# Kernel tuning notes

Measured on AMD Instinct MI355X. Metric: run time of the kernel, lower is better.

The kernel has to match this reference:

```python
import jax, jax.numpy as jnp
import numpy as np

HOP = 240  # subsample stride from torch.arange(239, T, 240)

def _causal_conv(x, w, b):
    # x: [B, Cin, T], w: [Cout, Cin, K], b: [Cout]
    pad = w.shape[-1] - 1
    xp = jnp.pad(x, ((0, 0), (0, 0), (pad, 0)))
    y = jax.lax.conv_general_dilated(xp, w, window_strides=(1,), padding='VALID',
                                     dimension_numbers=('NCW', 'OIW', 'NCW'))
    return y + b[None, :, None], xp[:, :, -pad:]

def _rvq(z, codebooks):
    # z: [B, T, D]; codebooks: [n, codebook_size, cd] with D = n*cd
    B, T, D = z.shape
    n, cs, cd = codebooks.shape
    zc = z.reshape(B, T, n, cd)
    r = zc[:, :, 0, :]
    qs, idxs = [], []
    for i in range(n):  # fixed small loop over 8 codebooks (sequential residual chain)
        cb = codebooks[i]  # [cs, cd]
        dist = (r ** 2).sum(-1, keepdims=True) + (cb ** 2).sum(-1) \
               - 2.0 * jnp.einsum('btd,cd->btc', r, cb)
        idx = jnp.argmin(dist, axis=-1)  # [B, T]
        q = cb[idx]                      # [B, T, cd]
        idxs.append(idx)
        qs.append(q)
        if i < n - 1:
            r = zc[:, :, i + 1, :] + (r - q)
    z_q = jnp.stack(qs, axis=2).reshape(B, T, D)
    return z_q, jnp.stack(idxs, axis=1)  # indices: [B, n, T]

def setup_inputs() -> dict:
    key = jax.random.key(0)
    ks = jax.random.split(key, 12)
    B, T = 4, 72000
    d_model = 512
    n_cb, cb_size, cb_dim = 8, 1024, d_model // 8
    s = 0.05
    return {
        'audio':   jax.random.normal(ks[0], (B, 1, T), dtype=jnp.float32),
        'conv1_w': jax.random.normal(ks[1], (64, 1, 7), dtype=jnp.float32) * s,
        'conv1_b': jnp.zeros((64,), dtype=jnp.float32),
        'conv2_w': jax.random.normal(ks[2], (128, 64, 5), dtype=jnp.float32) * s,
        'conv2_b': jnp.zeros((128,), dtype=jnp.float32),
        'conv3_w': jax.random.normal(ks[3], (256, 128, 5), dtype=jnp.float32) * s,
        'conv3_b': jnp.zeros((256,), dtype=jnp.float32),
        'conv4_w': jax.random.normal(ks[4], (d_model, 256, 3), dtype=jnp.float32) * s,
        'conv4_b': jnp.zeros((d_model,), dtype=jnp.float32),
        'codebooks': jax.random.normal(ks[5], (n_cb, cb_size, cb_dim), dtype=jnp.float32),
        'head_w': jax.random.normal(ks[6], (4, 64, d_model), dtype=jnp.float32) * s,
        'head_b': jnp.zeros((4, 64), dtype=jnp.float32),
    }

def reference(audio, conv1_w, conv1_b, conv2_w, conv2_b, conv3_w, conv3_b,
              conv4_w, conv4_b, codebooks, head_w, head_b):
    x, s1 = _causal_conv(audio, conv1_w, conv1_b); x = jax.nn.elu(x)
    x, s2 = _causal_conv(x, conv2_w, conv2_b);     x = jax.nn.elu(x)
    x, s3 = _causal_conv(x, conv3_w, conv3_b);     x = jax.nn.elu(x)
    x, s4 = _causal_conv(x, conv4_w, conv4_b);     x = jax.nn.elu(x)
    idx = jnp.arange(HOP - 1, x.shape[-1], HOP)
    x_sub = jnp.take(x, idx, axis=-1)              # [B, D, T_sub]
    z_q, a_tokens = _rvq(jnp.transpose(x_sub, (0, 2, 1)), codebooks)
    # b_logits: [B, 4, T_sub, 64]
    b_logits = jnp.einsum('btd,hod->bhto', z_q, head_w) + head_b[None, :, None, :]
    return a_tokens, b_logits, s1, s2, s3, s4
```

## Files before the change

kernel.cpp:

```cpp
#include <hip/hip_runtime.h>
#include <math.h>

#define HOP   240
#define T_IN  72000
#define NB    4
#define NF    300
#define NCB   8
#define CBS   1024
#define CBD   64

#define OFF_LOG 9600
#define OFF_S1  316800
#define OFF_S2  316824
#define OFF_S3  317848
#define OFF_S4  319896

#define WS_NRM   0
#define WS_W2P4  8192
#define WS_W3P4  49152
#define WS_W4P4  212992
#define WS_HW4   606208
#define WS_CBP4  737280
#define WS_TOTAL 1261568ull

__device__ __forceinline__ float elu1(float x) { return x > 0.f ? x : expm1f(x); }
__device__ __forceinline__ float dot4(float4 a, float4 b) {
    return a.x * b.x + a.y * b.y + a.z * b.z + a.w * b.w;
}
__device__ __forceinline__ float red16(float v) {
    v += __shfl_xor(v, 1); v += __shfl_xor(v, 2);
    v += __shfl_xor(v, 4); v += __shfl_xor(v, 8);
    return v;
}
__device__ __forceinline__ unsigned int fkey(float f) {
    unsigned int u = __float_as_uint(f);
    return (u & 0x80000000u) ? ~u : (u | 0x80000000u);
}

__global__ __launch_bounds__(256)
void prep_kernel(const float* __restrict__ w2, const float* __restrict__ w3,
                 const float* __restrict__ w4, const float* __restrict__ hw,
                 const float* __restrict__ cbs, float* __restrict__ wsf)
{
    const int bid = blockIdx.x;
    const float* src; float* dst;
    int R, L, I, K, tix, cx;
    bool do_norm = false;
    float* nrmp = nullptr;
    if (bid < 10)       { src = w2; dst = wsf + WS_W2P4; R = 128; L = 320; I = 64;  K = 5; tix = bid;       cx = 5;  }
    else if (bid < 50)  { src = w3; dst = wsf + WS_W3P4; R = 256; L = 640; I = 128; K = 5; tix = bid - 10;  cx = 10; }
    else if (bid < 146) { src = w4; dst = wsf + WS_W4P4; R = 512; L = 768; I = 256; K = 3; tix = bid - 50;  cx = 12; }
    else if (bid < 178) { src = hw; dst = wsf + WS_HW4;  R = 256; L = 512; I = 512; K = 1; tix = bid - 146; cx = 8;  }
    else {
        const int e = bid - 178, book = e >> 4;
        src = cbs + (size_t)book * 65536; dst = wsf + WS_CBP4 + (size_t)book * 65536;
        R = 1024; L = 64; I = 64; K = 1; tix = e & 15; cx = 1;
        do_norm = true; nrmp = wsf + WS_NRM + book * 1024;
    }
    const int c0 = (tix % cx) * 64, r0 = (tix / cx) * 64;
    const int lane = threadIdx.x & 63, q = threadIdx.x >> 6;

    __shared__ float tS[64][65];
    __shared__ float npart[4][64];

    #pragma unroll
    for (int i = 0; i < 16; ++i) {
        const int rr = q * 16 + i;
        tS[rr][lane] = src[(size_t)(r0 + rr) * L + c0 + lane];
    }
    __syncthreads();

    if (do_norm) {
        float s = 0.f;
        #pragma unroll
        for (int j = 0; j < 16; ++j) { const float v = tS[lane][q * 16 + j]; s += v * v; }
        npart[q][lane] = s;
        __syncthreads();
        if (threadIdx.x < 64)
            nrmp[r0 + threadIdx.x] = npart[0][threadIdx.x] + npart[1][threadIdx.x]
                                   + npart[2][threadIdx.x] + npart[3][threadIdx.x];
    }

    #pragma unroll
    for (int i = 0; i < 16; ++i) {
        const int col = c0 + q * 16 + i;
        const int dr = (K == 1) ? col : (col % K) * I + col / K;
        dst[((size_t)(dr >> 2) * R + (r0 + lane)) * 4 + (dr & 3)] = tS[lane][q * 16 + i];
    }
}

__global__ __launch_bounds__(512)
void mega_kernel(const float* __restrict__ audio,
                 const float* __restrict__ w1, const float* __restrict__ b1,
                 const float* __restrict__ b2, const float* __restrict__ b3,
                 const float* __restrict__ b4, const float* __restrict__ cbs,
                 const float* __restrict__ hb, const float* __restrict__ wsf,
                 float* __restrict__ out)
{
    const int blk = blockIdx.x;
    const int b   = blk / 60;
    const int f0  = (blk - b * 60) * 5;
    const int tid = threadIdx.x;
    const int lane = tid & 63, wid = tid >> 6;

    __shared__ float ashL[5][18];
    __shared__ __align__(16) float y1L[5 * 704];
    __shared__ __align__(16) float y2L[5 * 896];
    __shared__ __align__(16) float y3L[5 * 768];
    __shared__ __align__(16) float zsL[5 * 512];
    __shared__ __align__(16) float zqL[5 * 512];
    __shared__ __align__(16) float rs[320];
    __shared__ float redL[4480];
    __shared__ float rnS[5];
    __shared__ unsigned long long mk[2][5];

    if (tid < 85) {
        const int f = tid / 17, j = tid - (tid / 17) * 17;
        ashL[f][j] = audio[b * T_IN + (f0 + f) * HOP + 223 + j];
    }
    if (blk == 239 && tid < 6) out[OFF_S1 + 3 * 6 + tid] = audio[3 * T_IN + (T_IN - 6) + tid];
    __syncthreads();

    if (tid < 320) {
        const int f = tid >> 6, o = tid & 63;
        float wv[7];
        #pragma unroll
        for (int k = 0; k < 7; ++k) wv[k] = w1[o * 7 + k];
        const float bias = b1[o];
        float y1r[11];
        #pragma unroll
        for (int p = 0; p < 11; ++p) {
            float a = bias;
            #pragma unroll
            for (int k = 0; k < 7; ++k) a += wv[k] * ashL[f][p + k];
            y1r[p] = elu1(a);
            y1L[f * 704 + p * 64 + o] = y1r[p];
        }
        if (blk == 239 && f == 4) {
            #pragma unroll
            for (int j = 0; j < 4; ++j) out[OFF_S2 + 3 * 256 + o * 4 + j] = y1r[7 + j];
        }
    }
    __syncthreads();

    {
        const int c = tid & 127, h = (tid >> 7) & 1, g = tid >> 8;
        const int fb = g ? 3 : 0, nf = g ? 2 : 3;
        float acc[3][7];
        #pragma unroll
        for (int ff = 0; ff < 3; ++ff)
            #pragma unroll
            for (int p = 0; p < 7; ++p) acc[ff][p] = 0.f;

        const float4* wq = (const float4*)(wsf + WS_W2P4);
        for (int it = 0; it < 8; ++it) {
            const int itg = h * 8 + it;
            float4 wv[5];
            #pragma unroll
            for (int k = 0; k < 5; ++k) wv[k] = wq[(k * 16 + itg) * 128 + c];
            #pragma unroll
            for (int q = 0; q < 11; ++q) {
                float4 xv[3];
                #pragma unroll
                for (int ff = 0; ff < 3; ++ff)
                    if (ff < nf) xv[ff] = *(const float4*)&y1L[(fb + ff) * 704 + q * 64 + itg * 4];
                #pragma unroll
                for (int k = 0; k < 5; ++k) {
                    const int p = q - k;
                    if (p < 0 || p > 6) continue;
                    #pragma unroll
                    for (int ff = 0; ff < 3; ++ff)
                        if (ff < nf) acc[ff][p] += dot4(wv[k], xv[ff]);
                }
            }
        }
        if (h == 1) {
            #pragma unroll
            for (int ff = 0; ff < 3; ++ff)
                if (ff < nf)
                    #pragma unroll
                    for (int p = 0; p < 7; ++p)
                        redL[((fb + ff) * 7 + p) * 128 + c] = acc[ff][p];
        }
        __syncthreads();
        if (h == 0) {
            const float bias = b2[c];
            #pragma unroll
            for (int ff = 0; ff < 3; ++ff)
                if (ff < nf) {
                    const int f = fb + ff;
                    #pragma unroll
                    for (int p = 0; p < 7; ++p) {
                        const float v = elu1(acc[ff][p] + redL[(f * 7 + p) * 128 + c] + bias);
                        y2L[f * 896 + p * 128 + c] = v;
                        if (blk == 239 && f == 4 && p >= 3)
                            out[OFF_S3 + 3 * 512 + c * 4 + (p - 3)] = v;
                    }
                }
        }
        __syncthreads();
    }

    {
        const int c = tid & 255, h = tid >> 8;
        float acc[5][3];
        #pragma unroll
        for (int ff = 0; ff < 5; ++ff) { acc[ff][0] = acc[ff][1] = acc[ff][2] = 0.f; }

        const float4* wq = (const float4*)(wsf + WS_W3P4);
        for (int it = 0; it < 16; ++it) {
            const int itg = h * 16 + it;
            float4 wv[5];
            #pragma unroll
            for (int k = 0; k < 5; ++k) wv[k] = wq[(k * 32 + itg) * 256 + c];
            #pragma unroll
            for (int q = 0; q < 7; ++q) {
                float4 xv[5];
                #pragma unroll
                for (int ff = 0; ff < 5; ++ff)
                    xv[ff] = *(const float4*)&y2L[ff * 896 + q * 128 + itg * 4];
                #pragma unroll
                for (int k = 0; k < 5; ++k) {
                    const int p = q - k;
                    if (p < 0 || p > 2) continue;
                    #pragma unroll
                    for (int ff = 0; ff < 5; ++ff) acc[ff][p] += dot4(wv[k], xv[ff]);
                }
            }
        }
        if (h == 1) {
            #pragma unroll
            for (int ff = 0; ff < 5; ++ff)
                #pragma unroll
                for (int p = 0; p < 3; ++p) redL[(ff * 3 + p) * 256 + c] = acc[ff][p];
        }
        __syncthreads();
        if (h == 0) {
            const float bias = b3[c];
            #pragma unroll
            for (int ff = 0; ff < 5; ++ff)
                #pragma unroll
                for (int p = 0; p < 3; ++p) {
                    const float v = elu1(acc[ff][p] + redL[(ff * 3 + p) * 256 + c] + bias);
                    y3L[ff * 768 + p * 256 + c] = v;
                    if (blk == 239 && ff == 4 && p >= 1)
                        out[OFF_S4 + 3 * 512 + c * 2 + (p - 1)] = v;
                }
        }
        __syncthreads();
    }

    if (tid < 256) {
        const int c0 = tid, c1 = tid + 256;
        float a0[5], a1[5];
        #pragma unroll
        for (int ff = 0; ff < 5; ++ff) { a0[ff] = 0.f; a1[ff] = 0.f; }
        const float4* wq = (const float4*)(wsf + WS_W4P4);
        for (int rc = 0; rc < 192; ++rc) {
            const float4 w0 = wq[rc * 512 + c0];
            const float4 w1v = wq[rc * 512 + c1];
            #pragma unroll
            for (int ff = 0; ff < 5; ++ff) {
                const float4 xv = *(const float4*)&y3L[ff * 768 + rc * 4];
                a0[ff] += dot4(w0, xv);
                a1[ff] += dot4(w1v, xv);
            }
        }
        const float bi0 = b4[c0], bi1 = b4[c1];
        #pragma unroll
        for (int ff = 0; ff < 5; ++ff) {
            zsL[ff * 512 + c0] = elu1(a0[ff] + bi0);
            zsL[ff * 512 + c1] = elu1(a1[ff] + bi1);
        }
    }
    if (tid < 10) mk[tid / 5][tid % 5] = ~0ull;
    __syncthreads();

    if (tid < 320) {
        const float v = zsL[wid * 512 + lane];
        rs[tid] = v;
        float ss = v * v;
        #pragma unroll
        for (int m = 1; m < 64; m <<= 1) ss += __shfl_xor(ss, m);
        if (lane == 0) rnS[wid] = ss;
    }
    __syncthreads();

    const int c0 = tid << 1;
    for (int s = 0; s < NCB; ++s) {
        const float4* cbq = (const float4*)(wsf + WS_CBP4) + (size_t)s * 16384;
        float dA[5], dB[5];
        #pragma unroll
        for (int ff = 0; ff < 5; ++ff) { dA[ff] = 0.f; dB[ff] = 0.f; }

        for (int dc = 0; dc < 16; ++dc) {
            const float4 la = cbq[dc * 1024 + c0];
            const float4 lb = cbq[dc * 1024 + c0 + 1];
            #pragma unroll
            for (int ff = 0; ff < 5; ++ff) {
                const float4 rv = *(const float4*)&rs[ff * 64 + dc * 4];
                dA[ff] += dot4(la, rv);
                dB[ff] += dot4(lb, rv);
            }
        }
        const float2 nn = *(const float2*)(wsf + WS_NRM + s * CBS + c0);
        unsigned long long key[5];
        #pragma unroll
        for (int ff = 0; ff < 5; ++ff) {
            const float rn = rnS[ff];
            const float da = (rn + nn.x) - 2.f * dA[ff];
            const float db = (rn + nn.y) - 2.f * dB[ff];
            const unsigned long long ka = ((unsigned long long)fkey(da) << 32) | (unsigned)c0;
            const unsigned long long kb = ((unsigned long long)fkey(db) << 32) | (unsigned)(c0 + 1);
            key[ff] = ka < kb ? ka : kb;
        }
        #pragma unroll
        for (int m = 1; m < 64; m <<= 1) {
            #pragma unroll
            for (int ff = 0; ff < 5; ++ff) {
                const unsigned long long o = __shfl_xor(key[ff], m);
                if (o < key[ff]) key[ff] = o;
            }
        }
        if (lane == 0) {
            #pragma unroll
            for (int ff = 0; ff < 5; ++ff) atomicMin(&mk[s & 1][ff], key[ff]);
        }
        __syncthreads();

        if (tid < 5)
            out[b * (NCB * NF) + s * NF + (f0 + tid)]
                = (float)(unsigned)(mk[s & 1][tid] & 0xFFFFFFFFull);
        if (tid < 320) {
            const int idx = (int)(unsigned)(mk[s & 1][wid] & 0xFFFFFFFFull);
            const float qv = cbs[(size_t)(s * CBS + idx) * CBD + lane];
            zqL[wid * 512 + s * 64 + lane] = qv;
            if (s < NCB - 1) {
                const float nr = zsL[wid * 512 + (s + 1) * 64 + lane] + (rs[tid] - qv);
                rs[tid] = nr;
                float ss = nr * nr;
                #pragma unroll
                for (int m = 1; m < 64; m <<= 1) ss += __shfl_xor(ss, m);
                if (lane == 0) rnS[wid] = ss;
            }
        }
        if (tid >= 320 && tid < 325) mk[(s + 1) & 1][tid - 320] = ~0ull;
        __syncthreads();
    }

    {
        const int oc = tid & 255, h = tid >> 8;
        const float4* hq = (const float4*)(wsf + WS_HW4);
        float acc[5];
        #pragma unroll
        for (int ff = 0; ff < 5; ++ff) acc[ff] = 0.f;
        for (int rc = 0; rc < 64; ++rc) {
            const float4 wv = hq[(h * 64 + rc) * 256 + oc];
            #pragma unroll
            for (int ff = 0; ff < 5; ++ff) {
                const float4 xv = *(const float4*)&zqL[ff * 512 + h * 256 + rc * 4];
                acc[ff] += dot4(wv, xv);
            }
        }
        if (h == 1) {
            #pragma unroll
            for (int ff = 0; ff < 5; ++ff) redL[oc * 5 + ff] = acc[ff];
        }
        __syncthreads();
        if (h == 0) {
            const float bias = hb[oc];
            const int hh = oc >> 6, o = oc & 63;
            #pragma unroll
            for (int ff = 0; ff < 5; ++ff)
                out[OFF_LOG + ((size_t)(b * 4 + hh) * NF + (f0 + ff)) * 64 + o]
                    = acc[ff] + redL[oc * 5 + ff] + bias;
        }
    }
}

__global__ __launch_bounds__(256)
void enc_fused_kernel(const float* __restrict__ audio,
                      const float* __restrict__ w1, const float* __restrict__ b1,
                      const float* __restrict__ w2, const float* __restrict__ b2,
                      const float* __restrict__ w3, const float* __restrict__ b3,
                      const float* __restrict__ w4, const float* __restrict__ b4,
                      const float* __restrict__ cbs,
                      const float* __restrict__ hw, const float* __restrict__ hb,
                      float* __restrict__ out)
{
    const int tid = threadIdx.x;
    const int g = tid >> 4, sub = tid & 15, j0 = sub << 2;
    const int bf = blockIdx.x, b = bf / NF, f = bf - b * NF;
    const int t = f * HOP + (HOP - 1);

    __shared__ __align__(16) float ash[17];
    __shared__ __align__(16) float y1s[11 * 64];
    __shared__ __align__(16) float y2s[7 * 128];
    __shared__ __align__(16) float y3s[3 * 256];
    __shared__ __align__(16) float in_l[2240];
    __shared__ __align__(16) float zs[512];
    __shared__ __align__(16) float zqs[512];
    __shared__ __align__(16) float rsl[64];
    __shared__ float rdd[16]; __shared__ int rdi[16]; __shared__ int bidx_s;

    if (tid < 17) ash[tid] = audio[b * T_IN + (t - 16) + tid];
    __syncthreads();
    for (int j = tid; j < 11 * 64; j += 256) {
        const int p = j >> 6, o = j & 63;
        float acc = b1[o];
        for (int k = 0; k < 7; ++k) acc += w1[o * 7 + k] * ash[p + k];
        y1s[p * 64 + o] = elu1(acc);
    }
    __syncthreads();
    for (int j = tid; j < 7 * 320; j += 256) {
        const int p = j / 320, r = j - p * 320, i = r / 5, k = r - i * 5;
        in_l[j] = y1s[(p + k) * 64 + i];
    }
    __syncthreads();
    {
        float a[7];
        for (int ch = 0; ch < 8; ++ch) {
            const int c = g + (ch << 4);
            const float* wr = w2 + c * 320;
            for (int p = 0; p < 7; ++p) a[p] = 0.f;
            for (int st = 0; st < 5; ++st) {
                const float4 wv = *(const float4*)(wr + st * 64 + j0);
                for (int p = 0; p < 7; ++p)
                    a[p] += dot4(wv, *(const float4*)&in_l[p * 320 + st * 64 + j0]);
            }
            for (int p = 0; p < 7; ++p) a[p] = red16(a[p]);
            if (sub == 0) for (int p = 0; p < 7; ++p) y2s[p * 128 + c] = elu1(a[p] + b2[c]);
        }
    }
    __syncthreads();
    for (int j = tid; j < 3 * 640; j += 256) {
        const int p = j / 640, r = j - p * 640, i = r / 5, k = r - i * 5;
        in_l[j] = y2s[(p + k) * 128 + i];
    }
    __syncthreads();
    {
        float a[3];
        for (int ch = 0; ch < 16; ++ch) {
            const int c = g + (ch << 4);
            const float* wr = w3 + c * 640;
            a[0] = a[1] = a[2] = 0.f;
            for (int st = 0; st < 10; ++st) {
                const float4 wv = *(const float4*)(wr + st * 64 + j0);
                for (int p = 0; p < 3; ++p)
                    a[p] += dot4(wv, *(const float4*)&in_l[p * 640 + st * 64 + j0]);
            }
            for (int p = 0; p < 3; ++p) a[p] = red16(a[p]);
            if (sub == 0) for (int p = 0; p < 3; ++p) y3s[p * 256 + c] = elu1(a[p] + b3[c]);
        }
    }
    __syncthreads();
    for (int j = tid; j < 768; j += 256) { const int i = j / 3, k = j - i * 3; in_l[j] = y3s[k * 256 + i]; }
    __syncthreads();
    for (int ch = 0; ch < 32; ++ch) {
        const int c = g + (ch << 4);
        const float* wr = w4 + c * 768;
        float a = 0.f;
        for (int st = 0; st < 12; ++st)
            a += dot4(*(const float4*)(wr + st * 64 + j0), *(const float4*)&in_l[st * 64 + j0]);
        a = red16(a);
        if (sub == 0) zs[c] = elu1(a + b4[c]);
    }
    __syncthreads();
    if (tid < 64) rsl[tid] = zs[tid];
    __syncthreads();
    for (int s = 0; s < NCB; ++s) {
        const float* cb = cbs + s * (CBS * CBD);
        const float4 rv = *(const float4*)(rsl + j0);
        const float rn = red16(dot4(rv, rv));
        float bestd = 3.402823466e38f; int besti = 0;
        const int cc0 = g * 64;
        for (int cc = 0; cc < 64; ++cc) {
            const int c = cc0 + cc;
            const float4 cv = *(const float4*)(cb + c * CBD + j0);
            const float dt = red16(dot4(cv, rv));
            const float nnv = red16(dot4(cv, cv));
            const float d = rn + nnv - 2.f * dt;
            if (d < bestd) { bestd = d; besti = c; }
        }
        if (sub == 0) { rdd[g] = bestd; rdi[g] = besti; }
        __syncthreads();
        if (tid == 0) {
            float bd = rdd[0]; int bi = rdi[0];
            for (int q = 1; q < 16; ++q) if (rdd[q] < bd) { bd = rdd[q]; bi = rdi[q]; }
            bidx_s = bi;
            out[b * (NCB * NF) + s * NF + f] = (float)bi;
        }
        __syncthreads();
        const int idx = bidx_s;
        if (g == 0) {
            const float4 q4 = *(const float4*)(cb + idx * CBD + j0);
            *(float4*)&zqs[s * 64 + j0] = q4;
            if (s < NCB - 1) {
                const float4 zn = *(const float4*)&zs[(s + 1) * 64 + j0];
                float4 nr;
                nr.x = zn.x + (rv.x - q4.x); nr.y = zn.y + (rv.y - q4.y);
                nr.z = zn.z + (rv.z - q4.z); nr.w = zn.w + (rv.w - q4.w);
                *(float4*)&rsl[j0] = nr;
            }
        }
        __syncthreads();
    }
    for (int oo = 0; oo < 16; ++oo) {
        const int oc = g + (oo << 4);
        const float* wr = hw + oc * 512;
        float a = 0.f;
        for (int st = 0; st < 8; ++st)
            a += dot4(*(const float4*)(wr + st * 64 + j0), *(const float4*)&zqs[st * 64 + j0]);
        a = red16(a);
        if (sub == 0) {
            const int h = oc >> 6, o = oc & 63;
            out[OFF_LOG + ((b * 4 + h) * NF + f) * 64 + o] = a + hb[oc];
        }
    }
    if (f == NF - 1) {
        if (tid < 6) out[OFF_S1 + b * 6 + tid] = audio[b * T_IN + (T_IN - 6) + tid];
        out[OFF_S2 + b * 256 + tid] = y1s[(7 + (tid & 3)) * 64 + (tid >> 2)];
        for (int j = tid; j < 512; j += 256)
            out[OFF_S3 + b * 512 + j] = y2s[(3 + (j & 3)) * 128 + (j >> 2)];
        for (int j = tid; j < 512; j += 256)
            out[OFF_S4 + b * 512 + j] = y3s[(1 + (j & 1)) * 256 + (j >> 1)];
    }
}

extern "C" void kernel_launch(void* const* d_in, const int* in_sizes, int n_in,
                              void* d_out, int out_size, void* d_ws, size_t ws_size,
                              hipStream_t stream) {
    const float* audio = (const float*)d_in[0];
    const float* w1 = (const float*)d_in[1];
    const float* b1 = (const float*)d_in[2];
    const float* w2 = (const float*)d_in[3];
    const float* b2 = (const float*)d_in[4];
    const float* w3 = (const float*)d_in[5];
    const float* b3 = (const float*)d_in[6];
    const float* w4 = (const float*)d_in[7];
    const float* b4 = (const float*)d_in[8];
    const float* cbs = (const float*)d_in[9];
    const float* hw = (const float*)d_in[10];
    const float* hb = (const float*)d_in[11];
    float* out = (float*)d_out;
    float* wsf = (float*)d_ws;

    if (ws_size >= WS_TOTAL * sizeof(float)) {
        prep_kernel<<<dim3(306), 256, 0, stream>>>(w2, w3, w4, hw, cbs, wsf);
        mega_kernel<<<dim3(240), 512, 0, stream>>>(audio, w1, b1, b2, b3, b4,
                                                   cbs, hb, wsf, out);
    } else {
        enc_fused_kernel<<<dim3(NB * NF), 256, 0, stream>>>(
            audio, w1, b1, w2, b2, w3, b3, w4, b4, cbs, hw, hb, out);
    }
}
```

Before: 253.1 us.

## Shrink frames per block to three and rework prep weight repacking

```diff
diff --git a/kernel.cpp b/kernel.cpp
--- a/kernel.cpp
+++ b/kernel.cpp
@@ -44,52 +44,55 @@
 {
     const int bid = blockIdx.x;
     const float* src; float* dst;
-    int R, L, I, K, tix, cx;
-    bool do_norm = false;
-    float* nrmp = nullptr;
-    if (bid < 10)       { src = w2; dst = wsf + WS_W2P4; R = 128; L = 320; I = 64;  K = 5; tix = bid;       cx = 5;  }
-    else if (bid < 50)  { src = w3; dst = wsf + WS_W3P4; R = 256; L = 640; I = 128; K = 5; tix = bid - 10;  cx = 10; }
-    else if (bid < 146) { src = w4; dst = wsf + WS_W4P4; R = 512; L = 768; I = 256; K = 3; tix = bid - 50;  cx = 12; }
-    else if (bid < 178) { src = hw; dst = wsf + WS_HW4;  R = 256; L = 512; I = 512; K = 1; tix = bid - 146; cx = 8;  }
+    int C, I, K, c0, i0;
+    bool do_norm = false; float* nrmp = nullptr;
+    if (bid < 2)       { src = w2; dst = wsf + WS_W2P4; C = 128;  I = 64;  K = 5; c0 = bid * 64;        i0 = 0; }
+    else if (bid < 10) { const int e = bid - 2;  src = w3; dst = wsf + WS_W3P4; C = 256;  I = 128; K = 5; c0 = (e >> 1) * 64; i0 = (e & 1) * 64; }
+    else if (bid < 42) { const int e = bid - 10; src = w4; dst = wsf + WS_W4P4; C = 512;  I = 256; K = 3; c0 = (e >> 2) * 64; i0 = (e & 3) * 64; }
+    else if (bid < 74) { const int e = bid - 42; src = hw; dst = wsf + WS_HW4;  C = 256;  I = 512; K = 1; c0 = (e & 3) * 64;  i0 = (e >> 2) * 64; }
     else {
-        const int e = bid - 178, book = e >> 4;
+        const int e = bid - 74, book = e >> 4;
         src = cbs + (size_t)book * 65536; dst = wsf + WS_CBP4 + (size_t)book * 65536;
-        R = 1024; L = 64; I = 64; K = 1; tix = e & 15; cx = 1;
+        C = 1024; I = 64; K = 1; c0 = (e & 15) * 64; i0 = 0;
         do_norm = true; nrmp = wsf + WS_NRM + book * 1024;
     }
-    const int c0 = (tix % cx) * 64, r0 = (tix / cx) * 64;
+    const int L = I * K;
     const int lane = threadIdx.x & 63, q = threadIdx.x >> 6;
 
     __shared__ float tS[64][65];
     __shared__ float npart[4][64];
 
-    #pragma unroll
-    for (int i = 0; i < 16; ++i) {
-        const int rr = q * 16 + i;
-        tS[rr][lane] = src[(size_t)(r0 + rr) * L + c0 + lane];
-    }
-    __syncthreads();
-
-    if (do_norm) {
-        float s = 0.f;
-        #pragma unroll
-        for (int j = 0; j < 16; ++j) { const float v = tS[lane][q * 16 + j]; s += v * v; }
-        npart[q][lane] = s;
-        __syncthreads();
-        if (threadIdx.x < 64)
-            nrmp[r0 + threadIdx.x] = npart[0][threadIdx.x] + npart[1][threadIdx.x]
-                                   + npart[2][threadIdx.x] + npart[3][threadIdx.x];
-    }
-
-    #pragma unroll
-    for (int i = 0; i < 16; ++i) {
-        const int col = c0 + q * 16 + i;
-        const int dr = (K == 1) ? col : (col % K) * I + col / K;
-        dst[((size_t)(dr >> 2) * R + (r0 + lane)) * 4 + (dr & 3)] = tS[lane][q * 16 + i];
-    }
-}
-
-__global__ __launch_bounds__(512)
+    for (int k = 0; k < K; ++k) {
+        #pragma unroll
+        for (int r = 0; r < 16; ++r) {
+            const int cl = q * 16 + r;
+            tS[cl][lane] = src[(size_t)(c0 + cl) * L + (i0 + lane) * K + k];
+        }
+        __syncthreads();
+        if (do_norm && k == 0) {
+            float s = 0.f;
+            #pragma unroll
+            for (int j = 0; j < 16; ++j) { const float v = tS[lane][q * 16 + j]; s += v * v; }
+            npart[q][lane] = s;
+        }
+        #pragma unroll
+        for (int jj = 0; jj < 4; ++jj) {
+            const int j = q * 4 + jj;
+            float4 v;
+            v.x = tS[lane][4 * j + 0];
+            v.y = tS[lane][4 * j + 1];
+            v.z = tS[lane][4 * j + 2];
+            v.w = tS[lane][4 * j + 3];
+            ((float4*)dst)[(size_t)(k * (I >> 2) + (i0 >> 2) + j) * C + (c0 + lane)] = v;
+        }
+        __syncthreads();
+    }
+    if (do_norm && threadIdx.x < 64)
+        nrmp[c0 + threadIdx.x] = npart[0][threadIdx.x] + npart[1][threadIdx.x]
+                               + npart[2][threadIdx.x] + npart[3][threadIdx.x];
+}
+
+__global__ __launch_bounds__(512, 4)
 void mega_kernel(const float* __restrict__ audio,
                  const float* __restrict__ w1, const float* __restrict__ b1,
                  const float* __restrict__ b2, const float* __restrict__ b3,
@@ -98,30 +101,33 @@
                  float* __restrict__ out)
 {
     const int blk = blockIdx.x;
-    const int b   = blk / 60;
-    const int f0  = (blk - b * 60) * 5;
+    const int b   = blk / 100;
+    const int fi  = blk - b * 100;
+    const int f0  = fi * 3;
+    const bool tail = (fi == 99);
     const int tid = threadIdx.x;
     const int lane = tid & 63, wid = tid >> 6;
 
-    __shared__ float ashL[5][18];
-    __shared__ __align__(16) float y1L[5 * 704];
-    __shared__ __align__(16) float y2L[5 * 896];
-    __shared__ __align__(16) float y3L[5 * 768];
-    __shared__ __align__(16) float zsL[5 * 512];
-    __shared__ __align__(16) float zqL[5 * 512];
-    __shared__ __align__(16) float rs[320];
-    __shared__ float redL[4480];
-    __shared__ float rnS[5];
-    __shared__ unsigned long long mk[2][5];
-
-    if (tid < 85) {
-        const int f = tid / 17, j = tid - (tid / 17) * 17;
+    __shared__ float ashL[3][18];
+    __shared__ __align__(16) float y1L[3 * 704];
+    __shared__ __align__(16) float y2L[3 * 896];
+    __shared__ __align__(16) float y3L[3 * 768];
+    __shared__ __align__(16) float zsL[3 * 512];
+    __shared__ __align__(16) float zqL[3 * 512];
+    __shared__ __align__(16) float rs[192];
+    __shared__ float redL[2688];
+    __shared__ float rnS[3];
+    __shared__ unsigned long long mk[2][3];
+
+    if (tid < 51) {
+        const int f = tid / 17, j = tid - f * 17;
         ashL[f][j] = audio[b * T_IN + (f0 + f) * HOP + 223 + j];
     }
-    if (blk == 239 && tid < 6) out[OFF_S1 + 3 * 6 + tid] = audio[3 * T_IN + (T_IN - 6) + tid];
-    __syncthreads();
-
-    if (tid < 320) {
+    if (tail && tid < 6) out[OFF_S1 + b * 6 + tid] = audio[b * T_IN + (T_IN - 6) + tid];
+    if (tid < 6) mk[tid / 3][tid % 3] = ~0ull;
+    __syncthreads();
+
+    if (tid < 192) {
         const int f = tid >> 6, o = tid & 63;
         float wv[7];
         #pragma unroll
@@ -136,19 +142,19 @@
             y1r[p] = elu1(a);
             y1L[f * 704 + p * 64 + o] = y1r[p];
         }
-        if (blk == 239 && f == 4) {
-            #pragma unroll
-            for (int j = 0; j < 4; ++j) out[OFF_S2 + 3 * 256 + o * 4 + j] = y1r[7 + j];
+        if (tail && f == 2) {
+            #pragma unroll
+            for (int j = 0; j < 4; ++j) out[OFF_S2 + b * 256 + o * 4 + j] = y1r[7 + j];
         }
     }
     __syncthreads();
 
     {
         const int c = tid & 127, h = (tid >> 7) & 1, g = tid >> 8;
-        const int fb = g ? 3 : 0, nf = g ? 2 : 3;
-        float acc[3][7];
-        #pragma unroll
-        for (int ff = 0; ff < 3; ++ff)
+        const int fb = g * 2, nf = g ? 1 : 2;
+        float acc[2][7];
+        #pragma unroll
+        for (int ff = 0; ff < 2; ++ff)
             #pragma unroll
             for (int p = 0; p < 7; ++p) acc[ff][p] = 0.f;
 
@@ -160,23 +166,23 @@
             for (int k = 0; k < 5; ++k) wv[k] = wq[(k * 16 + itg) * 128 + c];
             #pragma unroll
             for (int q = 0; q < 11; ++q) {
-                float4 xv[3];
-                #pragma unroll
-                for (int ff = 0; ff < 3; ++ff)
+                float4 xv[2];
+                #pragma unroll
+                for (int ff = 0; ff < 2; ++ff)
                     if (ff < nf) xv[ff] = *(const float4*)&y1L[(fb + ff) * 704 + q * 64 + itg * 4];
                 #pragma unroll
                 for (int k = 0; k < 5; ++k) {
                     const int p = q - k;
                     if (p < 0 || p > 6) continue;
                     #pragma unroll
-                    for (int ff = 0; ff < 3; ++ff)
+                    for (int ff = 0; ff < 2; ++ff)
                         if (ff < nf) acc[ff][p] += dot4(wv[k], xv[ff]);
                 }
             }
         }
         if (h == 1) {
             #pragma unroll
-            for (int ff = 0; ff < 3; ++ff)
+            for (int ff = 0; ff < 2; ++ff)
                 if (ff < nf)
                     #pragma unroll
                     for (int p = 0; p < 7; ++p)
@@ -186,15 +192,15 @@
         if (h == 0) {
             const float bias = b2[c];
             #pragma unroll
-            for (int ff = 0; ff < 3; ++ff)
+            for (int ff = 0; ff < 2; ++ff)
                 if (ff < nf) {
                     const int f = fb + ff;
                     #pragma unroll
                     for (int p = 0; p < 7; ++p) {
                         const float v = elu1(acc[ff][p] + redL[(f * 7 + p) * 128 + c] + bias);
                         y2L[f * 896 + p * 128 + c] = v;
-                        if (blk == 239 && f == 4 && p >= 3)
-                            out[OFF_S3 + 3 * 512 + c * 4 + (p - 3)] = v;
+                        if (tail && f == 2 && p >= 3)
+                            out[OFF_S3 + b * 512 + c * 4 + (p - 3)] = v;
                     }
                 }
         }
@@ -203,9 +209,9 @@
 
     {
         const int c = tid & 255, h = tid >> 8;
-        float acc[5][3];
-        #pragma unroll
-        for (int ff = 0; ff < 5; ++ff) { acc[ff][0] = acc[ff][1] = acc[ff][2] = 0.f; }
+        float acc[3][3];
+        #pragma unroll
+        for (int ff = 0; ff < 3; ++ff) { acc[ff][0] = acc[ff][1] = acc[ff][2] = 0.f; }
 
         const float4* wq = (const float4*)(wsf + WS_W3P4);
         for (int it = 0; it < 16; ++it) {
@@ -215,22 +221,22 @@
             for (int k = 0; k < 5; ++k) wv[k] = wq[(k * 32 + itg) * 256 + c];
             #pragma unroll
             for (int q = 0; q < 7; ++q) {
-                float4 xv[5];
-                #pragma unroll
-                for (int ff = 0; ff < 5; ++ff)
+                float4 xv[3];
+                #pragma unroll
+                for (int ff = 0; ff < 3; ++ff)
                     xv[ff] = *(const float4*)&y2L[ff * 896 + q * 128 + itg * 4];
                 #pragma unroll
                 for (int k = 0; k < 5; ++k) {
                     const int p = q - k;
                     if (p < 0 || p > 2) continue;
                     #pragma unroll
-                    for (int ff = 0; ff < 5; ++ff) acc[ff][p] += dot4(wv[k], xv[ff]);
+                    for (int ff = 0; ff < 3; ++ff) acc[ff][p] += dot4(wv[k], xv[ff]);
                 }
             }
         }
         if (h == 1) {
             #pragma unroll
-            for (int ff = 0; ff < 5; ++ff)
+            for (int ff = 0; ff < 3; ++ff)
                 #pragma unroll
                 for (int p = 0; p < 3; ++p) redL[(ff * 3 + p) * 256 + c] = acc[ff][p];
         }
@@ -238,45 +244,38 @@
         if (h == 0) {
             const float bias = b3[c];
             #pragma unroll
-            for (int ff = 0; ff < 5; ++ff)
+            for (int ff = 0; ff < 3; ++ff)
                 #pragma unroll
                 for (int p = 0; p < 3; ++p) {
                     const float v = elu1(acc[ff][p] + redL[(ff * 3 + p) * 256 + c] + bias);
                     y3L[ff * 768 + p * 256 + c] = v;
-                    if (blk == 239 && ff == 4 && p >= 1)
-                        out[OFF_S4 + 3 * 512 + c * 2 + (p - 1)] = v;
+                    if (tail && ff == 2 && p >= 1)
+                        out[OFF_S4 + b * 512 + c * 2 + (p - 1)] = v;
                 }
         }
         __syncthreads();
     }
 
-    if (tid < 256) {
-        const int c0 = tid, c1 = tid + 256;
-        float a0[5], a1[5];
-        #pragma unroll
-        for (int ff = 0; ff < 5; ++ff) { a0[ff] = 0.f; a1[ff] = 0.f; }
+    {
+        const int c = tid;
+        float acc[3] = {0.f, 0.f, 0.f};
         const float4* wq = (const float4*)(wsf + WS_W4P4);
         for (int rc = 0; rc < 192; ++rc) {
-            const float4 w0 = wq[rc * 512 + c0];
-            const float4 w1v = wq[rc * 512 + c1];
-            #pragma unroll
-            for (int ff = 0; ff < 5; ++ff) {
+            const float4 w0 = wq[rc * 512 + c];
+            #pragma unroll
+            for (int ff = 0; ff < 3; ++ff) {
                 const float4 xv = *(const float4*)&y3L[ff * 768 + rc * 4];
-                a0[ff] += dot4(w0, xv);
-                a1[ff] += dot4(w1v, xv);
-            }
-        }
-        const float bi0 = b4[c0], bi1 = b4[c1];
-        #pragma unroll
-        for (int ff = 0; ff < 5; ++ff) {
-            zsL[ff * 512 + c0] = elu1(a0[ff] + bi0);
-            zsL[ff * 512 + c1] = elu1(a1[ff] + bi1);
-        }
-    }
-    if (tid < 10) mk[tid / 5][tid % 5] = ~0ull;
-    __syncthreads();
-
-    if (tid < 320) {
+                acc[ff] += dot4(w0, xv);
+            }
+        }
+        const float bias = b4[c];
+        #pragma unroll
+        for (int ff = 0; ff < 3; ++ff)
+            zsL[ff * 512 + c] = elu1(acc[ff] + bias);
+    }
+    __syncthreads();
+
+    if (tid < 192) {
         const float v = zsL[wid * 512 + lane];
         rs[tid] = v;
         float ss = v * v;
@@ -289,24 +288,24 @@
     const int c0 = tid << 1;
     for (int s = 0; s < NCB; ++s) {
         const float4* cbq = (const float4*)(wsf + WS_CBP4) + (size_t)s * 16384;
-        float dA[5], dB[5];
-        #pragma unroll
-        for (int ff = 0; ff < 5; ++ff) { dA[ff] = 0.f; dB[ff] = 0.f; }
+        float dA[3], dB[3];
+        #pragma unroll
+        for (int ff = 0; ff < 3; ++ff) { dA[ff] = 0.f; dB[ff] = 0.f; }
 
         for (int dc = 0; dc < 16; ++dc) {
             const float4 la = cbq[dc * 1024 + c0];
             const float4 lb = cbq[dc * 1024 + c0 + 1];
             #pragma unroll
-            for (int ff = 0; ff < 5; ++ff) {
+            for (int ff = 0; ff < 3; ++ff) {
                 const float4 rv = *(const float4*)&rs[ff * 64 + dc * 4];
                 dA[ff] += dot4(la, rv);
                 dB[ff] += dot4(lb, rv);
             }
         }
         const float2 nn = *(const float2*)(wsf + WS_NRM + s * CBS + c0);
-        unsigned long long key[5];
-        #pragma unroll
-        for (int ff = 0; ff < 5; ++ff) {
+        unsigned long long key[3];
+        #pragma unroll
+        for (int ff = 0; ff < 3; ++ff) {
             const float rn = rnS[ff];
             const float da = (rn + nn.x) - 2.f * dA[ff];
             const float db = (rn + nn.y) - 2.f * dB[ff];
@@ -317,21 +316,21 @@
         #pragma unroll
         for (int m = 1; m < 64; m <<= 1) {
             #pragma unroll
-            for (int ff = 0; ff < 5; ++ff) {
+            for (int ff = 0; ff < 3; ++ff) {
                 const unsigned long long o = __shfl_xor(key[ff], m);
                 if (o < key[ff]) key[ff] = o;
             }
         }
         if (lane == 0) {
             #pragma unroll
-            for (int ff = 0; ff < 5; ++ff) atomicMin(&mk[s & 1][ff], key[ff]);
-        }
-        __syncthreads();
-
-        if (tid < 5)
+            for (int ff = 0; ff < 3; ++ff) atomicMin(&mk[s & 1][ff], key[ff]);
+        }
+        __syncthreads();
+
+        if (tid < 3)
             out[b * (NCB * NF) + s * NF + (f0 + tid)]
                 = (float)(unsigned)(mk[s & 1][tid] & 0xFFFFFFFFull);
-        if (tid < 320) {
+        if (tid < 192) {
             const int idx = (int)(unsigned)(mk[s & 1][wid] & 0xFFFFFFFFull);
             const float qv = cbs[(size_t)(s * CBS + idx) * CBD + lane];
             zqL[wid * 512 + s * 64 + lane] = qv;
@@ -344,36 +343,34 @@
                 if (lane == 0) rnS[wid] = ss;
             }
         }
-        if (tid >= 320 && tid < 325) mk[(s + 1) & 1][tid - 320] = ~0ull;
+        if (tid >= 192 && tid < 195) mk[(s + 1) & 1][tid - 192] = ~0ull;
         __syncthreads();
     }
 
     {
         const int oc = tid & 255, h = tid >> 8;
         const float4* hq = (const float4*)(wsf + WS_HW4);
-        float acc[5];
-        #pragma unroll
-        for (int ff = 0; ff < 5; ++ff) acc[ff] = 0.f;
+        float acc[3] = {0.f, 0.f, 0.f};
         for (int rc = 0; rc < 64; ++rc) {
             const float4 wv = hq[(h * 64 + rc) * 256 + oc];
             #pragma unroll
-            for (int ff = 0; ff < 5; ++ff) {
+            for (int ff = 0; ff < 3; ++ff) {
                 const float4 xv = *(const float4*)&zqL[ff * 512 + h * 256 + rc * 4];
                 acc[ff] += dot4(wv, xv);
             }
         }
         if (h == 1) {
             #pragma unroll
-            for (int ff = 0; ff < 5; ++ff) redL[oc * 5 + ff] = acc[ff];
+            for (int ff = 0; ff < 3; ++ff) redL[oc * 3 + ff] = acc[ff];
         }
         __syncthreads();
         if (h == 0) {
             const float bias = hb[oc];
             const int hh = oc >> 6, o = oc & 63;
             #pragma unroll
-            for (int ff = 0; ff < 5; ++ff)
+            for (int ff = 0; ff < 3; ++ff)
                 out[OFF_LOG + ((size_t)(b * 4 + hh) * NF + (f0 + ff)) * 64 + o]
-                    = acc[ff] + redL[oc * 5 + ff] + bias;
+                    = acc[ff] + redL[oc * 3 + ff] + bias;
         }
     }
 }
@@ -546,8 +543,8 @@
     float* wsf = (float*)d_ws;
 
     if (ws_size >= WS_TOTAL * sizeof(float)) {
-        prep_kernel<<<dim3(306), 256, 0, stream>>>(w2, w3, w4, hw, cbs, wsf);
-        mega_kernel<<<dim3(240), 512, 0, stream>>>(audio, w1, b1, b2, b3, b4,
+        prep_kernel<<<dim3(202), 256, 0, stream>>>(w2, w3, w4, hw, cbs, wsf);
+        mega_kernel<<<dim3(400), 512, 0, stream>>>(audio, w1, b1, b2, b3, b4,
                                                    cbs, hb, wsf, out);
     } else {
         enc_fused_kernel<<<dim3(NB * NF), 256, 0, stream>>>(
```

Measured after the change: 245.3 us. -3.1%, faster.
